# Optimization experiments

Measured on AMD Instinct MI355X. Metric: run time of the kernel, lower is better.

Reference implementation:

```python
import jax, jax.numpy as jnp
import numpy as np

DIM = 256
HEADS = 8
G = 8            # group (window) size per axis
POS_DIM = 16     # (dim // 4) // 4
MLP_HIDDEN = 4 * DIM


def layernorm(x, g, b, eps=1e-5):
    m = x.mean(-1, keepdims=True)
    v = ((x - m) ** 2).mean(-1, keepdims=True)
    return (x - m) / jnp.sqrt(v + eps) * g + b


def setup_inputs() -> dict:
    key = jax.random.key(0)
    ks = jax.random.split(key, 32)
    s = 0.02
    d = {}
    d['x'] = jax.random.normal(ks[0], (1, 32768, DIM), jnp.float32)
    d['y'] = jax.random.normal(ks[1], (1, 32768, DIM), jnp.float32)
    d['n1_g'] = jnp.ones((DIM,), jnp.float32)
    d['n1_b'] = jnp.zeros((DIM,), jnp.float32)
    d['qkv_w'] = jax.random.normal(ks[2], (DIM, 3 * DIM), jnp.float32) * s
    d['qkv_b'] = jnp.zeros((3 * DIM,), jnp.float32)
    d['pp_w'] = jax.random.normal(ks[3], (3, POS_DIM), jnp.float32) * s
    d['pp_b'] = jnp.zeros((POS_DIM,), jnp.float32)
    d['p1_lng'] = jnp.ones((POS_DIM,), jnp.float32)
    d['p1_lnb'] = jnp.zeros((POS_DIM,), jnp.float32)
    d['p1_w'] = jax.random.normal(ks[4], (POS_DIM, POS_DIM), jnp.float32) * s
    d['p1_b'] = jnp.zeros((POS_DIM,), jnp.float32)
    d['p2_lng'] = jnp.ones((POS_DIM,), jnp.float32)
    d['p2_lnb'] = jnp.zeros((POS_DIM,), jnp.float32)
    d['p2_w'] = jax.random.normal(ks[5], (POS_DIM, POS_DIM), jnp.float32) * s
    d['p2_b'] = jnp.zeros((POS_DIM,), jnp.float32)
    d['p3_lng'] = jnp.ones((POS_DIM,), jnp.float32)
    d['p3_lnb'] = jnp.zeros((POS_DIM,), jnp.float32)
    d['p3_w'] = jax.random.normal(ks[6], (POS_DIM, HEADS), jnp.float32) * s
    d['p3_b'] = jnp.zeros((HEADS,), jnp.float32)
    d['proj_w'] = jax.random.normal(ks[7], (DIM, DIM), jnp.float32) * s
    d['proj_b'] = jnp.zeros((DIM,), jnp.float32)
    d['n2_g'] = jnp.ones((DIM,), jnp.float32)
    d['n2_b'] = jnp.zeros((DIM,), jnp.float32)
    d['fc1_w'] = jax.random.normal(ks[8], (DIM, MLP_HIDDEN), jnp.float32) * s
    d['fc1_b'] = jnp.zeros((MLP_HIDDEN,), jnp.float32)
    d['fc2_w'] = jax.random.normal(ks[9], (MLP_HIDDEN, DIM), jnp.float32) * s
    d['fc2_b'] = jnp.zeros((DIM,), jnp.float32)
    d['H'] = 32
    d['W'] = 32
    d['D'] = 32
    return d


def reference(x, y, n1_g, n1_b, qkv_w, qkv_b, pp_w, pp_b,
              p1_lng, p1_lnb, p1_w, p1_b, p2_lng, p2_lnb, p2_w, p2_b,
              p3_lng, p3_lnb, p3_w, p3_b, proj_w, proj_b,
              n2_g, n2_b, fc1_w, fc1_b, fc2_w, fc2_b, H, W, D):
    B, L, C = x.shape
    nh, g = HEADS, G
    hd = C // nh
    shortcut = x
    xn = layernorm(x, n1_g, n1_b)
    xv = xn.reshape(B, H, W, D, C)
    yv = y.reshape(B, H, W, D, C)  # note: y is NOT normed in the original

    # SDA window partition (H,W,D divisible by g -> no padding, zero mask)
    def part(t):
        t = t.reshape(B, H // g, g, W // g, g, D // g, g, C)
        t = t.transpose(0, 1, 3, 5, 2, 4, 6, 7)
        return t.reshape(-1, g * g * g, C)

    xg, yg = part(xv), part(yv)
    B_, N, _ = xg.shape

    # original quirk: self.qkv used for BOTH x and y (qkv_y layer unused)
    qkv = (xg @ qkv_w + qkv_b).reshape(B_, N, 3, nh, hd).transpose(2, 0, 3, 1, 4)
    qkv_y = (yg @ qkv_w + qkv_b).reshape(B_, N, 3, nh, hd).transpose(2, 0, 3, 1, 4)
    q = qkv[0] * (hd ** -0.5)
    k_y, v_y = qkv_y[1], qkv_y[2]

    attn = jnp.einsum('bhnd,bhmd->bhnm', q, k_y)  # [B_, nh, N, N]

    # dynamic relative position bias (small MLP + gather)
    rng = jnp.arange(1 - g, g)
    bh, bw, bd = jnp.meshgrid(rng, rng, rng, indexing='ij')
    biases = jnp.stack([bh, bw, bd], -1).reshape(-1, 3).astype(x.dtype)  # [(2g-1)^3, 3]
    pos = biases @ pp_w + pp_b
    pos = jax.nn.relu(layernorm(pos, p1_lng, p1_lnb)) @ p1_w + p1_b
    pos = jax.nn.relu(layernorm(pos, p2_lng, p2_lnb)) @ p2_w + p2_b
    pos = jax.nn.relu(layernorm(pos, p3_lng, p3_lnb)) @ p3_w + p3_b  # [(2g-1)^3, nh]

    c = jnp.arange(g)
    ch, cw, cd = jnp.meshgrid(c, c, c, indexing='ij')
    cf = jnp.stack([ch, cw, cd], 0).reshape(3, -1)          # [3, g^3]
    rel = (cf[:, :, None] - cf[:, None, :]).transpose(1, 2, 0) + (g - 1)
    idx = rel[..., 0] * (2 * g - 1) * (2 * g - 1) + rel[..., 1] * (2 * g - 1) + rel[..., 2]
    bias = pos[idx].transpose(2, 0, 1)  # [nh, N, N]

    attn = jax.nn.softmax(attn + bias[None], axis=-1)
    out = jnp.einsum('bhnm,bhmd->bhnd', attn, v_y).transpose(0, 2, 1, 3).reshape(B_, N, C)
    out = out @ proj_w + proj_b

    # reverse window partition
    out = out.reshape(B, H // g, W // g, D // g, g, g, g, C)
    out = out.transpose(0, 1, 4, 2, 5, 3, 6, 7).reshape(B, H * W * D, C)

    x = shortcut + out
    x2 = layernorm(x, n2_g, n2_b)
    h = jax.nn.gelu(x2 @ fc1_w + fc1_b, approximate=False)
    x = x + (h @ fc2_w + fc2_b)
    return x
```

## Files before the change

### kernel.cpp

```cpp
#include <hip/hip_runtime.h>
#include <cstdint>
#include <cstddef>

typedef unsigned int u32;
typedef unsigned short u16;
typedef __attribute__((ext_vector_type(8))) short bf16x8;
typedef __attribute__((ext_vector_type(4))) float f32x4;

#define DEV __device__ __forceinline__

DEV u16 f2b(float f){ u32 x = __float_as_uint(f); x += 0x7fffu + ((x>>16)&1u); return (u16)(x>>16); }
DEV u32 pk2(float a, float b){
  u32 r;
  asm("v_cvt_pk_bf16_f32 %0, %1, %2" : "=v"(r) : "v"(a), "v"(b));
  return r;
}

DEV void gll16(const void* g, void* l){
  __builtin_amdgcn_global_load_lds((const __attribute__((address_space(1))) u32*)g,
                                   (__attribute__((address_space(3))) u32*)l, 16, 0, 0);
}

DEV void win_n(int r, int& win, int& n){
  int d_ = r & 31, w_ = (r>>5)&31, h_ = r>>10;
  win = ((h_>>3)<<4) | ((w_>>3)<<2) | (d_>>3);
  n   = ((h_&7)<<6)  | ((w_&7)<<3)  | (d_&7);
}
DEV int tok_of(int r){
  int win = r>>9, nn = r&511;
  int bh = win>>4, bw=(win>>2)&3, bd=win&3;
  int ih = nn>>6,  iw=(nn>>3)&7,  id=nn&7;
  return ((bh*8+ih)<<10) | ((bw*8+iw)<<5) | (bd*8+id);
}


__global__ void wtrall_k(const float* __restrict__ qkv_w, const float* __restrict__ proj_w,
                         const float* __restrict__ fc1_w, const float* __restrict__ fc2_w,
                         u16* __restrict__ qkvT, u16* __restrict__ projT,
                         u16* __restrict__ fc1T, u16* __restrict__ fc2T){
  int f = blockIdx.x*256 + threadIdx.x;
  const float* w; u16* wt; int g; bool k10 = false; int N;
  if (f < 196608)      { w=qkv_w;  wt=qkvT;  g=f;        N=768;  }
  else if (f < 262144) { w=proj_w; wt=projT; g=f-196608; N=256;  }
  else if (f < 524288) { w=fc1_w;  wt=fc1T;  g=f-262144; N=1024; }
  else                 { w=fc2_w;  wt=fc2T;  g=f-524288; N=256;  k10=true; }
  int n = k10 ? (g>>10) : (g>>8);
  int k = k10 ? (g&1023) : (g&255);
  wt[g] = f2b(w[(size_t)k*N + n]);
}

__global__ void conv_k(const float* __restrict__ x, u16* __restrict__ o, int n4){
  int stride = gridDim.x*blockDim.x;
  for (int i = blockIdx.x*blockDim.x + threadIdx.x; i < n4; i += stride){
    const float4 v = *(const float4*)(x + (size_t)i*4);
    u32 lo = (u32)f2b(v.x) | ((u32)f2b(v.y)<<16);
    u32 hi = (u32)f2b(v.z) | ((u32)f2b(v.w)<<16);
    *(uint2*)(o + (size_t)i*4) = make_uint2(lo, hi);
  }
}

__global__ __launch_bounds__(256)
void ln_k(const float* __restrict__ x, const float* __restrict__ g,
          const float* __restrict__ b, u16* __restrict__ out){
  int row  = blockIdx.x*4 + (threadIdx.x>>6);
  int lane = threadIdx.x & 63;
  const float4 v = *(const float4*)(x + (size_t)row*256 + lane*4);
  float s = v.x+v.y+v.z+v.w;
  #pragma unroll
  for (int m=1;m<64;m<<=1) s += __shfl_xor(s, m);
  float mean = s * (1.0f/256.0f);
  float d0=v.x-mean,d1=v.y-mean,d2=v.z-mean,d3=v.w-mean;
  float q = d0*d0+d1*d1+d2*d2+d3*d3;
  #pragma unroll
  for (int m=1;m<64;m<<=1) q += __shfl_xor(q, m);
  float rs = rsqrtf(q*(1.0f/256.0f) + 1e-5f);
  const float4 gg = *(const float4*)(g + lane*4);
  const float4 bb = *(const float4*)(b + lane*4);
  u32 lo = (u32)f2b(d0*rs*gg.x+bb.x) | ((u32)f2b(d1*rs*gg.y+bb.y)<<16);
  u32 hi = (u32)f2b(d2*rs*gg.z+bb.z) | ((u32)f2b(d3*rs*gg.w+bb.w)<<16);
  *(uint2*)(out + (size_t)row*256 + lane*4) = make_uint2(lo,hi);
}

template<int NOUT>
DEV void pstage(float* v, const float* g, const float* b, const float* W, const float* bb){
  float m = 0.f;
  #pragma unroll
  for (int i=0;i<16;i++) m += v[i];
  m *= 0.0625f;
  float q = 0.f;
  #pragma unroll
  for (int i=0;i<16;i++){ float d=v[i]-m; q += d*d; }
  float rs = rsqrtf(q*0.0625f + 1e-5f);
  float u[16];
  #pragma unroll
  for (int i=0;i<16;i++){ float t = (v[i]-m)*rs*g[i] + b[i]; u[i] = t>0.f?t:0.f; }
  #pragma unroll
  for (int o=0;o<NOUT;o++){
    float s = bb[o];
    #pragma unroll
    for (int kk=0;kk<16;kk++) s += u[kk]*W[kk*NOUT+o];
    v[o] = s;
  }
}

__global__ void posmlp_k(const float* pp_w, const float* pp_b,
                         const float* g1, const float* b1, const float* w1, const float* bb1,
                         const float* g2, const float* b2, const float* w2, const float* bb2,
                         const float* g3, const float* b3, const float* w3, const float* bb3,
                         float* __restrict__ posb){
  int i = blockIdx.x*256 + threadIdx.x;
  if (i >= 3375) return;
  int t = i;
  int bd = t % 15; t /= 15;
  int bw = t % 15; t /= 15;
  int bh = t;
  float fh = (float)(bh-7), fw = (float)(bw-7), fd = (float)(bd-7);
  float v[16];
  #pragma unroll
  for (int o=0;o<16;o++) v[o] = fh*pp_w[o] + fw*pp_w[16+o] + fd*pp_w[32+o] + pp_b[o];
  pstage<16>(v, g1,b1,w1,bb1);
  pstage<16>(v, g2,b2,w2,bb2);
  pstage<8> (v, g3,b3,w3,bb3);
  #pragma unroll
  for (int h=0;h<8;h++) posb[(size_t)h*3376 + i] = v[h] * 1.4426950408889634f;
}

struct GemmP {
  const u16* A; const u16* Bt;
  int K;
  const float* bvec;
  float scale;
  const float* add32;
  float* out32;
  u16* out16;
  u16* out16b;
};

template<int MODE>
DEV void epi(const GemmP& p, int r, int c, float val){
  if constexpr (MODE==0){
    float qv = (val + p.bvec[c]) * p.scale;
    int win, n; win_n(r, win, n);
    int hh = c>>5, dd = c&31;
    p.out16[((size_t)((win*8+hh)*512 + n)<<5) + dd] = f2b(qv);
  } else if constexpr (MODE==1){
    float ov = val + p.bvec[c];
    int win, n; win_n(r, win, n);
    int cc = c & 255;
    int hh = cc>>5, dd = cc&31;
    size_t base = (size_t)(win*8+hh)*16384;
    if (c < 256){
      int nc = n>>4, ln2 = ((dd>>3)<<4)|(n&15), jj = dd&7;
      p.out16[base + (size_t)(nc*64+ln2)*8 + jj] = f2b(ov);
    } else {
      int fi = ((n>>5)<<1) | (dd>>4);
      int ln2 = (((n>>3)&3)<<4)|(dd&15), jj = n&7;
      p.out16b[base + (size_t)(fi*64+ln2)*8 + jj] = f2b(ov);
    }
  } else if constexpr (MODE==2){
    int l = tok_of(r);
    size_t o = (size_t)l*256 + c;
    p.out32[o] = val + p.bvec[c] + p.add32[o];
  } else if constexpr (MODE==3){
    float u = val + p.bvec[c];
    float ge = 0.5f*u*(1.0f + erff(u*0.70710678118654752f));
    p.out16[(size_t)r*1024 + c] = f2b(ge);
  } else {
    size_t o = (size_t)r*256 + c;
    p.out32[o] = val + p.bvec[c] + p.add32[o];
  }
}

template<int MODE, int NT>
__global__ __launch_bounds__(256)
void gemmA_k(GemmP p){
  __shared__ u16 lA[8][2048];
  __shared__ u16 lB[2][4096];
  const int tid = threadIdx.x;
  const int wid = tid>>6, lane = tid&63;
  const int lr = lane&15, lg = lane>>4;
  const int m0 = blockIdx.x*64;
  const int wm = (wid>>1)*32, wn = (wid&1)*64;
  const f32x4 z4 = {0.f,0.f,0.f,0.f};

  #pragma unroll
  for (int it=0; it<8; ++it){
    int off = (it*256 + tid)*16;
    int kt  = off>>12;
    int row = (off>>6)&63;
    int kcol = kt*32 + ((off&63)>>1);
    const u16* ga;
    if constexpr (MODE==2){
      int rr = m0+row;
      ga = p.A + ((size_t)((rr>>9)*8 + (kcol>>5))*512 + (rr&511))*32 + (kcol&31);
    } else {
      ga = p.A + (size_t)(m0+row)*256 + kcol;
    }
    gll16(ga, (char*)lA + off);
  }
  auto stageB = [&](int buf, int t){
    int j = t>>3, kt = t&7;
    #pragma unroll
    for (int r=0;r<2;r++){
      int off = (r*256 + tid)*16;
      int row = off>>6;
      gll16(p.Bt + (size_t)(j*128+row)*256 + kt*32 + ((off&63)>>1), (char*)lB[buf] + off);
    }
  };
  stageB(0, 0);
  int cur = 0;

  f32x4 acc[2][4];
  #pragma unroll
  for (int i=0;i<2;i++)
    #pragma unroll
    for (int j=0;j<4;j++) acc[i][j] = z4;

  for (int t=0; t<NT*8; ++t){
    const int kt = t&7;
    if (t+1 < NT*8){
      stageB(cur^1, t+1);
      asm volatile("s_waitcnt vmcnt(2)" ::: "memory");
    } else {
      asm volatile("s_waitcnt vmcnt(0)" ::: "memory");
    }
    __builtin_amdgcn_s_barrier();
    __builtin_amdgcn_sched_barrier(0);
    bf16x8 af[2], bfr[4];
    #pragma unroll
    for (int i=0;i<2;i++)
      af[i]  = *(const bf16x8*)&lA[kt][(wm + i*16 + lr)*32 + lg*8];
    #pragma unroll
    for (int j=0;j<4;j++)
      bfr[j] = *(const bf16x8*)&lB[cur][(wn + j*16 + lr)*32 + lg*8];
    #pragma unroll
    for (int i=0;i<2;i++)
      #pragma unroll
      for (int j=0;j<4;j++)
        acc[i][j] = __builtin_amdgcn_mfma_f32_16x16x32_bf16(af[i], bfr[j], acc[i][j], 0,0,0);
    __builtin_amdgcn_sched_barrier(0);
    if (kt == 7){
      int n0 = (t>>3)*128;
      #pragma unroll
      for (int i=0;i<2;i++)
        #pragma unroll
        for (int j=0;j<4;j++){
          #pragma unroll
          for (int v=0;v<4;v++)
            epi<MODE>(p, m0 + wm + i*16 + lg*4 + v, n0 + wn + j*16 + lr, acc[i][j][v]);
          acc[i][j] = z4;
        }
      if (t+1 < NT*8) __syncthreads();
    } else {
      __builtin_amdgcn_s_barrier();
    }
    cur ^= 1;
  }
}

__global__ __launch_bounds__(256)
void gemmW_k(GemmP p){
  __shared__ u16 lA[2][2048];
  __shared__ u16 lB[2][8192];
  const int tid = threadIdx.x;
  const int wid = tid>>6, lane = tid&63;
  const int lr = lane&15, lg = lane>>4;
  const int m0 = blockIdx.x*64;
  const int wm = (wid>>1)*32, wn = (wid&1)*128;
  const f32x4 z4 = {0.f,0.f,0.f,0.f};

  auto stage = [&](int buf, int kt){
    int offA = tid*16;
    int rowA = offA>>6;
    gll16(p.A + (size_t)(m0+rowA)*1024 + kt*32 + ((offA&63)>>1), (char*)lA[buf] + offA);
    #pragma unroll
    for (int r=0;r<4;r++){
      int off = (r*256 + tid)*16;
      int row = off>>6;
      gll16(p.Bt + (size_t)row*1024 + kt*32 + ((off&63)>>1), (char*)lB[buf] + off);
    }
  };
  stage(0, 0);
  int cur = 0;

  f32x4 acc[2][8];
  #pragma unroll
  for (int i=0;i<2;i++)
    #pragma unroll
    for (int j=0;j<8;j++) acc[i][j] = z4;

  for (int kt=0; kt<32; ++kt){
    if (kt+1 < 32){
      stage(cur^1, kt+1);
      asm volatile("s_waitcnt vmcnt(5)" ::: "memory");
    } else {
      asm volatile("s_waitcnt vmcnt(0)" ::: "memory");
    }
    __builtin_amdgcn_s_barrier();
    __builtin_amdgcn_sched_barrier(0);
    bf16x8 af[2], bfr[8];
    #pragma unroll
    for (int i=0;i<2;i++)
      af[i]  = *(const bf16x8*)&lA[cur][(wm + i*16 + lr)*32 + lg*8];
    #pragma unroll
    for (int j=0;j<8;j++)
      bfr[j] = *(const bf16x8*)&lB[cur][(wn + j*16 + lr)*32 + lg*8];
    #pragma unroll
    for (int i=0;i<2;i++)
      #pragma unroll
      for (int j=0;j<8;j++)
        acc[i][j] = __builtin_amdgcn_mfma_f32_16x16x32_bf16(af[i], bfr[j], acc[i][j], 0,0,0);
    __builtin_amdgcn_sched_barrier(0);
    if (kt+1 < 32) __builtin_amdgcn_s_barrier();
    cur ^= 1;
  }

  #pragma unroll
  for (int i=0;i<2;i++)
    #pragma unroll
    for (int j=0;j<8;j++)
      #pragma unroll
      for (int v=0;v<4;v++)
        epi<4>(p, m0 + wm + i*16 + lg*4 + v, wn + j*16 + lr, acc[i][j][v]);
}

__global__ __launch_bounds__(512, 2)
void attn_k(const u16* __restrict__ Q, const u16* __restrict__ Kf,
            const u16* __restrict__ Vf, const float* __restrict__ posb,
            u16* __restrict__ outF){
  __shared__ u16 lK[16384];
  __shared__ u16 lV[16384];
  __shared__ float lPf[3392];
  const int bid = blockIdx.x;
  const int hh = bid&7;
  const int tid = threadIdx.x, wid = tid>>6, lane = tid&63;
  const int lr = lane&15, lg = lane>>4;
  const u16* Kb = Kf + (size_t)bid*16384;
  const u16* Vb = Vf + (size_t)bid*16384;
  const u16* Qb = Q  + (size_t)bid*16384;
  #pragma unroll
  for (int r=0;r<4;r++){
    int off = (r*512 + tid)*16;
    gll16((const char*)Kb + off, (char*)lK + off);
    gll16((const char*)Vb + off, (char*)lV + off);
  }
  const float* ptab = posb + (size_t)hh*3376;
  for (int t=tid; t<3375; t+=512) lPf[t] = ptab[t];
  __syncthreads();
  const f32x4 z4 = {0.f,0.f,0.f,0.f};

  for (int ch=0; ch<4; ++ch){
    const int r0 = wid*64 + ch*16;
    const int q  = r0 + lr;
    const int Ab = (q>>6)*225 + ((q>>3)&7)*15 + (q&7) + 1687 - (lg>>1)*15 - (lg&1)*4;
    bf16x8 qf = *(const bf16x8*)(Qb + (size_t)q*32 + lg*8);
    f32x4 o0 = z4, o1 = z4;
    float sv0 = 0.f, sv1 = 0.f, sv2 = 0.f, sv3 = 0.f;
    #pragma unroll
    for (int ph=0; ph<2; ++ph){
      f32x4 sf[16];
      __builtin_amdgcn_s_setprio(1);
      #pragma unroll
      for (int i=0;i<16;i++){
        int nc = ph*16 + i;
        bf16x8 kf = *(const bf16x8*)&lK[(nc*64 + lane)*8];
        sf[i] = __builtin_amdgcn_mfma_f32_16x16x32_bf16(kf, qf, z4, 0,0,0);
      }
      __builtin_amdgcn_s_setprio(0);
      #pragma unroll
      for (int i=0;i<16;i++){
        int nc = ph*16 + i;
        const float* bp = lPf + (Ab - (nc>>2)*225 - (nc&3)*30 - 3);
        float e3 = exp2f(sf[i][3] + bp[0]);
        float e2 = exp2f(sf[i][2] + bp[1]);
        float e1 = exp2f(sf[i][1] + bp[2]);
        float e0 = exp2f(sf[i][0] + bp[3]);
        sf[i][0]=e0; sf[i][1]=e1; sf[i][2]=e2; sf[i][3]=e3;
        sv0 += e0; sv1 += e1; sv2 += e2; sv3 += e3;
      }
      #pragma unroll
      for (int kc=0;kc<8;kc++){
        u32 a0 = pk2(sf[2*kc  ][0], sf[2*kc  ][1]);
        u32 a1 = pk2(sf[2*kc  ][2], sf[2*kc  ][3]);
        u32 b0 = pk2(sf[2*kc+1][0], sf[2*kc+1][1]);
        u32 b1 = pk2(sf[2*kc+1][2], sf[2*kc+1][3]);
        asm("v_permlane32_swap_b32 %0, %1" : "+v"(a0), "+v"(b0));
        asm("v_permlane16_swap_b32 %0, %1" : "+v"(a0), "+v"(b0));
        asm("v_permlane32_swap_b32 %0, %1" : "+v"(a1), "+v"(b1));
        asm("v_permlane16_swap_b32 %0, %1" : "+v"(a1), "+v"(b1));
        bf16x8 pf;
        ((u32*)&pf)[0]=a0; ((u32*)&pf)[1]=a1; ((u32*)&pf)[2]=b0; ((u32*)&pf)[3]=b1;
        int kcg = ph*8 + kc;
        bf16x8 v0 = *(const bf16x8*)&lV[(size_t)((kcg*2+0)*64 + lane)*8];
        bf16x8 v1 = *(const bf16x8*)&lV[(size_t)((kcg*2+1)*64 + lane)*8];
        __builtin_amdgcn_s_setprio(1);
        o0 = __builtin_amdgcn_mfma_f32_16x16x32_bf16(pf, v0, o0, 0,0,0);
        o1 = __builtin_amdgcn_mfma_f32_16x16x32_bf16(pf, v1, o1, 0,0,0);
        __builtin_amdgcn_s_setprio(0);
      }
    }
    float s = (sv0+sv1) + (sv2+sv3);
    s += __shfl_xor(s,16);
    s += __shfl_xor(s,32);
    #pragma unroll
    for (int v=0;v<4;v++){
      float inv = 1.0f / __shfl(s, lg*4+v);
      int n = r0 + lg*4 + v;
      size_t base = ((size_t)bid*512 + n)*32;
      outF[base + lr]      = f2b(o0[v]*inv);
      outF[base + 16 + lr] = f2b(o1[v]*inv);
    }
  }
}

extern "C" void kernel_launch(void* const* d_in, const int* in_sizes, int n_in,
                              void* d_out, int out_size, void* d_ws, size_t ws_size,
                              hipStream_t stream){
  const float* x      = (const float*)d_in[0];
  const float* y      = (const float*)d_in[1];
  const float* n1_g   = (const float*)d_in[2];
  const float* n1_b   = (const float*)d_in[3];
  const float* qkv_w  = (const float*)d_in[4];
  const float* qkv_b  = (const float*)d_in[5];
  const float* pp_w   = (const float*)d_in[6];
  const float* pp_b   = (const float*)d_in[7];
  const float* p1_lng = (const float*)d_in[8];
  const float* p1_lnb = (const float*)d_in[9];
  const float* p1_w   = (const float*)d_in[10];
  const float* p1_b   = (const float*)d_in[11];
  const float* p2_lng = (const float*)d_in[12];
  const float* p2_lnb = (const float*)d_in[13];
  const float* p2_w   = (const float*)d_in[14];
  const float* p2_b   = (const float*)d_in[15];
  const float* p3_lng = (const float*)d_in[16];
  const float* p3_lnb = (const float*)d_in[17];
  const float* p3_w   = (const float*)d_in[18];
  const float* p3_b   = (const float*)d_in[19];
  const float* proj_w = (const float*)d_in[20];
  const float* proj_b = (const float*)d_in[21];
  const float* n2_g   = (const float*)d_in[22];
  const float* n2_b   = (const float*)d_in[23];
  const float* fc1_w  = (const float*)d_in[24];
  const float* fc1_b  = (const float*)d_in[25];
  const float* fc2_w  = (const float*)d_in[26];
  const float* fc2_b  = (const float*)d_in[27];
  float* out = (float*)d_out;
  char* ws = (char*)d_ws;

  u16*   qkvT  = (u16*)  (ws + 0);
  u16*   projT = (u16*)  (ws + 393216);
  u16*   fc1T  = (u16*)  (ws + 524288);
  u16*   fc2T  = (u16*)  (ws + 1048576);
  float* posb  = (float*)(ws + 1572864);
  u16*   xn    = (u16*)  (ws + 5898240);
  u16*   yb    = (u16*)  (ws + 22675456);
  u16*   Qb    = (u16*)  (ws + 39452672);
  u16*   Kfb   = (u16*)  (ws + 56229888);
  u16*   Vfb   = (u16*)  (ws + 73007104);
  u16*   attnF = (u16*)  (ws + 89784320);
  float* xres  = (float*)(ws + 106561536);
  u16*   hbuf  = xn;
  u16*   x2n   = attnF;

  wtrall_k<<<3072,256,0,stream>>>(qkv_w, proj_w, fc1_w, fc2_w, qkvT, projT, fc1T, fc2T);
  posmlp_k<<<14,256,0,stream>>>(pp_w, pp_b,
                                p1_lng,p1_lnb,p1_w,p1_b,
                                p2_lng,p2_lnb,p2_w,p2_b,
                                p3_lng,p3_lnb,p3_w,p3_b, posb);
  ln_k<<<8192,256,0,stream>>>(x, n1_g, n1_b, xn);
  conv_k<<<2048,256,0,stream>>>(y, yb, 2097152);

  GemmP pq; pq.A=xn; pq.Bt=qkvT; pq.K=256; pq.bvec=qkv_b;
  pq.scale=0.17677669529663687f*1.4426950408889634f;
  pq.add32=nullptr; pq.out32=nullptr; pq.out16=Qb; pq.out16b=nullptr;
  gemmA_k<0,2><<<512,256,0,stream>>>(pq);

  GemmP pkv; pkv.A=yb; pkv.Bt=qkvT + 256*256; pkv.K=256; pkv.bvec=qkv_b + 256;
  pkv.scale=1.f; pkv.add32=nullptr; pkv.out32=nullptr; pkv.out16=Kfb; pkv.out16b=Vfb;
  gemmA_k<1,4><<<512,256,0,stream>>>(pkv);

  attn_k<<<512,512,0,stream>>>(Qb, Kfb, Vfb, posb, attnF);

  GemmP pp; pp.A=attnF; pp.Bt=projT; pp.K=256; pp.bvec=proj_b;
  pp.scale=1.f; pp.add32=x; pp.out32=xres; pp.out16=nullptr; pp.out16b=nullptr;
  gemmA_k<2,2><<<512,256,0,stream>>>(pp);

  ln_k<<<8192,256,0,stream>>>(xres, n2_g, n2_b, x2n);

  GemmP pf1; pf1.A=x2n; pf1.Bt=fc1T; pf1.K=256; pf1.bvec=fc1_b;
  pf1.scale=1.f; pf1.add32=nullptr; pf1.out32=nullptr; pf1.out16=hbuf; pf1.out16b=nullptr;
  gemmA_k<3,8><<<512,256,0,stream>>>(pf1);

  GemmP pf2; pf2.A=hbuf; pf2.Bt=fc2T; pf2.K=1024; pf2.bvec=fc2_b;
  pf2.scale=1.f; pf2.add32=xres; pf2.out32=out; pf2.out16=nullptr; pf2.out16b=nullptr;
  gemmW_k<<<512,256,0,stream>>>(pf2);
}
```

Measured before the change: 284.1 us.

## Triple-buffer GEMM B/A tiles and store LDS in MFMA fragment order

Both GEMM kernels move from double to triple buffering. The next-next stage load is issued after the MFMA block, which removes the second barrier per k-step and lets loads run two iterations ahead. LDS tiles are also rewritten so each wave loads 16x32 fragments laid out in lane order (lane*16 bytes). This makes the fragment reads contiguous and avoids bank conflicts. The cost is extra LDS per block (one more buffer), which may lower occupancy, and the wait counts have to line up with the new outstanding-load count.

```diff
diff --git a/kernel.cpp b/kernel.cpp
--- a/kernel.cpp
+++ b/kernel.cpp
@@ -174,41 +174,40 @@
 template<int MODE, int NT>
 __global__ __launch_bounds__(256)
 void gemmA_k(GemmP p){
-  __shared__ u16 lA[8][2048];
-  __shared__ u16 lB[2][4096];
+  __shared__ u16 lA[16384];
+  __shared__ u16 lB[3][4096];
   const int tid = threadIdx.x;
   const int wid = tid>>6, lane = tid&63;
   const int lr = lane&15, lg = lane>>4;
   const int m0 = blockIdx.x*64;
   const int wm = (wid>>1)*32, wn = (wid&1)*64;
+  const int T = NT*8;
   const f32x4 z4 = {0.f,0.f,0.f,0.f};
 
   #pragma unroll
   for (int it=0; it<8; ++it){
-    int off = (it*256 + tid)*16;
-    int kt  = off>>12;
-    int row = (off>>6)&63;
-    int kcol = kt*32 + ((off&63)>>1);
+    int f = it*4 + wid;
+    int rt = f>>3, kt = f&7;
+    int row = m0 + rt*16 + lr;
     const u16* ga;
     if constexpr (MODE==2){
-      int rr = m0+row;
-      ga = p.A + ((size_t)((rr>>9)*8 + (kcol>>5))*512 + (rr&511))*32 + (kcol&31);
+      ga = p.A + ((size_t)((row>>9)*8 + kt)*512 + (row&511))*32 + lg*8;
     } else {
-      ga = p.A + (size_t)(m0+row)*256 + kcol;
-    }
-    gll16(ga, (char*)lA + off);
+      ga = p.A + (size_t)row*256 + kt*32 + lg*8;
+    }
+    gll16(ga, (char*)lA + f*1024 + lane*16);
   }
   auto stageB = [&](int buf, int t){
     int j = t>>3, kt = t&7;
     #pragma unroll
     for (int r=0;r<2;r++){
-      int off = (r*256 + tid)*16;
-      int row = off>>6;
-      gll16(p.Bt + (size_t)(j*128+row)*256 + kt*32 + ((off&63)>>1), (char*)lB[buf] + off);
+      int f = r*4 + wid;
+      gll16(p.Bt + (size_t)(j*128 + f*16 + lr)*256 + kt*32 + lg*8,
+            (char*)lB[buf] + f*1024 + lane*16);
     }
   };
   stageB(0, 0);
-  int cur = 0;
+  if (T > 1) stageB(1, 1);
 
   f32x4 acc[2][4];
   #pragma unroll
@@ -216,23 +215,24 @@
     #pragma unroll
     for (int j=0;j<4;j++) acc[i][j] = z4;
 
-  for (int t=0; t<NT*8; ++t){
+  int cur = 0, stg = 2;
+  for (int t=0; t<T; ++t){
     const int kt = t&7;
-    if (t+1 < NT*8){
-      stageB(cur^1, t+1);
-      asm volatile("s_waitcnt vmcnt(2)" ::: "memory");
-    } else {
-      asm volatile("s_waitcnt vmcnt(0)" ::: "memory");
-    }
+    if (t+1 < T) asm volatile("s_waitcnt vmcnt(2)" ::: "memory");
+    else         asm volatile("s_waitcnt vmcnt(0)" ::: "memory");
     __builtin_amdgcn_s_barrier();
     __builtin_amdgcn_sched_barrier(0);
     bf16x8 af[2], bfr[4];
     #pragma unroll
-    for (int i=0;i<2;i++)
-      af[i]  = *(const bf16x8*)&lA[kt][(wm + i*16 + lr)*32 + lg*8];
-    #pragma unroll
-    for (int j=0;j<4;j++)
-      bfr[j] = *(const bf16x8*)&lB[cur][(wn + j*16 + lr)*32 + lg*8];
+    for (int i=0;i<2;i++){
+      int fA = ((wid>>1)*2 + i)*8 + kt;
+      af[i] = *(const bf16x8*)((const char*)lA + fA*1024 + lane*16);
+    }
+    #pragma unroll
+    for (int j=0;j<4;j++){
+      int fB = (wid&1)*4 + j;
+      bfr[j] = *(const bf16x8*)((const char*)lB[cur] + fB*1024 + lane*16);
+    }
     #pragma unroll
     for (int i=0;i<2;i++)
       #pragma unroll
@@ -250,18 +250,17 @@
             epi<MODE>(p, m0 + wm + i*16 + lg*4 + v, n0 + wn + j*16 + lr, acc[i][j][v]);
           acc[i][j] = z4;
         }
-      if (t+1 < NT*8) __syncthreads();
-    } else {
-      __builtin_amdgcn_s_barrier();
-    }
-    cur ^= 1;
+    }
+    if (t+2 < T) stageB(stg, t+2);
+    cur = (cur==2)?0:cur+1;
+    stg = (stg==2)?0:stg+1;
   }
 }
 
 __global__ __launch_bounds__(256)
 void gemmW_k(GemmP p){
-  __shared__ u16 lA[2][2048];
-  __shared__ u16 lB[2][8192];
+  __shared__ u16 lA[3][2048];
+  __shared__ u16 lB[3][8192];
   const int tid = threadIdx.x;
   const int wid = tid>>6, lane = tid&63;
   const int lr = lane&15, lg = lane>>4;
@@ -270,18 +269,17 @@
   const f32x4 z4 = {0.f,0.f,0.f,0.f};
 
   auto stage = [&](int buf, int kt){
-    int offA = tid*16;
-    int rowA = offA>>6;
-    gll16(p.A + (size_t)(m0+rowA)*1024 + kt*32 + ((offA&63)>>1), (char*)lA[buf] + offA);
+    gll16(p.A + (size_t)(m0 + wid*16 + lr)*1024 + kt*32 + lg*8,
+          (char*)lA[buf] + wid*1024 + lane*16);
     #pragma unroll
     for (int r=0;r<4;r++){
-      int off = (r*256 + tid)*16;
-      int row = off>>6;
-      gll16(p.Bt + (size_t)row*1024 + kt*32 + ((off&63)>>1), (char*)lB[buf] + off);
+      int f = r*4 + wid;
+      gll16(p.Bt + (size_t)(f*16 + lr)*1024 + kt*32 + lg*8,
+            (char*)lB[buf] + f*1024 + lane*16);
     }
   };
   stage(0, 0);
-  int cur = 0;
+  stage(1, 1);
 
   f32x4 acc[2][8];
   #pragma unroll
@@ -289,30 +287,32 @@
     #pragma unroll
     for (int j=0;j<8;j++) acc[i][j] = z4;
 
+  int cur = 0, stg = 2;
   for (int kt=0; kt<32; ++kt){
-    if (kt+1 < 32){
-      stage(cur^1, kt+1);
-      asm volatile("s_waitcnt vmcnt(5)" ::: "memory");
-    } else {
-      asm volatile("s_waitcnt vmcnt(0)" ::: "memory");
-    }
+    if (kt+1 < 32) asm volatile("s_waitcnt vmcnt(5)" ::: "memory");
+    else           asm volatile("s_waitcnt vmcnt(0)" ::: "memory");
     __builtin_amdgcn_s_barrier();
     __builtin_amdgcn_sched_barrier(0);
     bf16x8 af[2], bfr[8];
     #pragma unroll
-    for (int i=0;i<2;i++)
-      af[i]  = *(const bf16x8*)&lA[cur][(wm + i*16 + lr)*32 + lg*8];
-    #pragma unroll
-    for (int j=0;j<8;j++)
-      bfr[j] = *(const bf16x8*)&lB[cur][(wn + j*16 + lr)*32 + lg*8];
+    for (int i=0;i<2;i++){
+      int fA = (wid>>1)*2 + i;
+      af[i] = *(const bf16x8*)((const char*)lA[cur] + fA*1024 + lane*16);
+    }
+    #pragma unroll
+    for (int j=0;j<8;j++){
+      int fB = (wid&1)*8 + j;
+      bfr[j] = *(const bf16x8*)((const char*)lB[cur] + fB*1024 + lane*16);
+    }
     #pragma unroll
     for (int i=0;i<2;i++)
       #pragma unroll
       for (int j=0;j<8;j++)
         acc[i][j] = __builtin_amdgcn_mfma_f32_16x16x32_bf16(af[i], bfr[j], acc[i][j], 0,0,0);
     __builtin_amdgcn_sched_barrier(0);
-    if (kt+1 < 32) __builtin_amdgcn_s_barrier();
-    cur ^= 1;
+    if (kt+2 < 32) stage(stg, kt+2);
+    cur = (cur==2)?0:cur+1;
+    stg = (stg==2)?0:stg+1;
   }
 
   #pragma unroll
```

New measurement: 292.5 us. 1.03x slower.
